# Kernel optimization log

Measured on AMD Instinct MI355X. Metric: run time of the kernel, lower is better.

## Reference

```python
import jax, jax.numpy as jnp
import numpy as np

B, T, C, HS = 4, 2048, 1024, 128

def setup_inputs() -> dict:
    key = jax.random.key(0)
    k0, k1, k2, k3 = jax.random.split(key, 4)
    scale = 1.0 / np.sqrt(C)
    return {
        "x": jax.random.normal(k0, (B, T, C), dtype=jnp.float32),
        "Wk": jax.random.normal(k1, (C, HS), dtype=jnp.float32) * scale,
        "Wq": jax.random.normal(k2, (C, HS), dtype=jnp.float32) * scale,
        "Wv": jax.random.normal(k3, (C, HS), dtype=jnp.float32) * scale,
    }

def reference(x, Wk, Wq, Wv):
    # k, q, v: [B, T, HS]
    k = jnp.einsum('btc,ch->bth', x, Wk)
    q = jnp.einsum('btc,ch->bth', x, Wq)
    v = jnp.einsum('btc,ch->bth', x, Wv)
    hs = k.shape[-1]
    # full T x T scores (no causal mask in source), scaled by head_size**-0.5
    wei = jnp.einsum('bqh,bkh->bqk', q, k) * (hs ** -0.5)
    wei = jax.nn.softmax(wei, axis=-1)
    # dropout p=0.0 -> identity
    out = jnp.einsum('bqk,bkh->bqh', wei, v)
    return out
```

## Files before the change

### kernel.cpp

```cpp
#include <hip/hip_runtime.h>
#include <hip/hip_bf16.h>

typedef float  f32x4  __attribute__((ext_vector_type(4)));
typedef float  f32x8  __attribute__((ext_vector_type(8)));
typedef float  f32x16 __attribute__((ext_vector_type(16)));
typedef short  s4v    __attribute__((ext_vector_type(4)));
typedef short  s8v    __attribute__((ext_vector_type(8)));
typedef __bf16 b4v    __attribute__((ext_vector_type(4)));
typedef __bf16 b8v    __attribute__((ext_vector_type(8)));
typedef unsigned int u32;
typedef unsigned short ushort;

#define T_DIM  2048
#define C_DIM  1024


typedef const __attribute__((address_space(1))) u32 gu32;
typedef __attribute__((address_space(3))) u32 lu32;

static __device__ __forceinline__ void glds16(const void* g, void* l) {
  __builtin_amdgcn_global_load_lds((gu32*)g, (lu32*)l, 16, 0, 0);
}

static __device__ __forceinline__ b8v ldb8(const ushort* p) {
  return __builtin_bit_cast(b8v, *reinterpret_cast<const s8v*>(p));
}

static __device__ __forceinline__ b4v cvt4(f32x4 v) {
  b4v r;
#pragma unroll
  for (int i = 0; i < 4; ++i) r[i] = (__bf16)v[i];
  return r;
}

static __device__ __forceinline__ ushort bfu(float f) {
  __bf16 h = (__bf16)f;
  return __builtin_bit_cast(ushort, h);
}

static __device__ __forceinline__ f32x16 mfma32(b8v a, b8v b, f32x16 c) {
  return __builtin_amdgcn_mfma_f32_32x32x16_bf16(a, b, c, 0, 0, 0);
}

#define BAR_VM(N)                                                        \
  asm volatile("s_waitcnt vmcnt(" #N ") lgkmcnt(0)" ::: "memory");       \
  __builtin_amdgcn_s_barrier();                                          \
  asm volatile("" ::: "memory");

__global__ __launch_bounds__(256) void wconv(const float* __restrict__ Wq,
                                             const float* __restrict__ Wk,
                                             const float* __restrict__ Wv,
                                             ushort* __restrict__ Wt) {
  __shared__ float lds[32][65];
  const int m  = blockIdx.z;
  const int c0 = blockIdx.x * 32;
  const int h0 = blockIdx.y * 64;
  const float* W = (m == 0) ? Wq : (m == 1) ? Wk : Wv;

  const int cl = threadIdx.x >> 3;
  const int h8 = (threadIdx.x & 7) * 8;
  {
    float4 a = *reinterpret_cast<const float4*>(W + (c0 + cl) * 128 + h0 + h8);
    float4 b =
        *reinterpret_cast<const float4*>(W + (c0 + cl) * 128 + h0 + h8 + 4);
    lds[cl][h8] = a.x; lds[cl][h8 + 1] = a.y;
    lds[cl][h8 + 2] = a.z; lds[cl][h8 + 3] = a.w;
    lds[cl][h8 + 4] = b.x; lds[cl][h8 + 5] = b.y;
    lds[cl][h8 + 6] = b.z; lds[cl][h8 + 7] = b.w;
  }
  __syncthreads();
  const int hl = threadIdx.x >> 2;
  const int cs = (threadIdx.x & 3) * 8;
  s8v o;
#pragma unroll
  for (int i = 0; i < 8; ++i) o[i] = (short)bfu(lds[cs + i][hl]);
  *reinterpret_cast<s8v*>(Wt + (m * 128 + h0 + hl) * C_DIM + c0 + cs) = o;
}

__global__ __launch_bounds__(512) void proj(const float* __restrict__ x,
                                            const ushort* __restrict__ Wt,
                                            ushort* __restrict__ q,
                                            ushort* __restrict__ k,
                                            ushort* __restrict__ vt) {
  __shared__ __align__(16) ushort Ab[2][32 * 72];
  __shared__ __align__(16) ushort Bb[2][128 * 64];
  float* red = (float*)&Bb[0][0];
  ushort* stage = &Bb[1][0];

  const int t   = threadIdx.x;
  const int w   = t >> 6;
  const int lid = t & 63;
  const int hi  = lid >> 5;
  const int ln  = lid & 31;
  const int ks  = w >> 2;
  const int nc  = w & 3;
  const int m   = blockIdx.y;
  const int r0  = blockIdx.x * 32;

  const int arow = t >> 4;
  const int acol = (t & 15) * 4;
  const float* ag = x + (r0 + arow) * C_DIM + acol;

  const int bswz = (((lid & 7) ^ (lid >> 3)) << 4);
  const char* bg = (const char*)(Wt + m * 128 * C_DIM);

  f32x16 acc[2] = {};

#define PROJ_BSTAGE(KK, BUF)                                              \
  _Pragma("unroll") for (int j = 0; j < 2; ++j) {                         \
    int h = j * 64 + w * 8 + (lid >> 3);                                  \
    glds16(bg + h * 2048 + (KK) * 2 + bswz,                               \
           (char*)&Bb[BUF][0] + j * 8192 + w * 1024);                     \
  }

  f32x4 av = *reinterpret_cast<const f32x4*>(ag);
  PROJ_BSTAGE(0, 0)
  {
    b4v ac = cvt4(av);
    *reinterpret_cast<s4v*>(&Ab[0][arow * 72 + acol]) =
        __builtin_bit_cast(s4v, ac);
  }
  __syncthreads();

  int cur = 0;
#pragma unroll 1
  for (int i = 0; i < 16; ++i) {
    const int nxt = cur ^ 1;
    f32x4 an;
    if (i < 15) {
      const int kk = (i + 1) * 64;
      PROJ_BSTAGE(kk, nxt)
      an = *reinterpret_cast<const f32x4*>(ag + kk);
    }

    const int h = nc * 32 + ln;
#pragma unroll
    for (int c = 0; c < 2; ++c) {
      const int s = ks * 2 + c;
      b8v af = ldb8(&Ab[cur][ln * 72 + s * 16 + hi * 8]);
      int inner = ((s * 2 + hi) << 4) ^ ((h & 7) << 4);
      b8v bf =
          ldb8((const ushort*)((const char*)&Bb[cur][0] + h * 128 + inner));
      __builtin_amdgcn_s_setprio(1);
      acc[c] = mfma32(af, bf, acc[c]);
      __builtin_amdgcn_s_setprio(0);
    }

    if (i < 15) {
      b4v anc = cvt4(an);
      *reinterpret_cast<s4v*>(&Ab[nxt][arow * 72 + acol]) =
          __builtin_bit_cast(s4v, anc);
    }
    __syncthreads();
    cur = nxt;
  }
#undef PROJ_BSTAGE

  f32x16 fa = acc[0] + acc[1];

  if (ks == 1) {
#pragma unroll
    for (int r = 0; r < 16; ++r) {
      int qm = (r & 3) + 8 * (r >> 2) + 4 * hi;
      red[(nc * 32 + qm) * 32 + ln] = fa[r];
    }
  }
  __syncthreads();
  if (ks == 0) {
#pragma unroll
    for (int r = 0; r < 16; ++r) {
      int qm = (r & 3) + 8 * (r >> 2) + 4 * hi;
      fa[r] += red[(nc * 32 + qm) * 32 + ln];
    }
    if (m < 2) {
#pragma unroll
      for (int r = 0; r < 16; ++r) {
        int row = (r & 3) + 8 * (r >> 2) + 4 * hi;
        stage[row * 136 + nc * 32 + ln] = bfu(fa[r]);
      }
    } else {
#pragma unroll
      for (int r = 0; r < 16; ++r) {
        int trow = (r & 3) + 8 * (r >> 2) + 4 * hi;
        stage[(nc * 32 + ln) * 40 + trow] = bfu(fa[r]);
      }
    }
  }
  __syncthreads();

  if (m < 2) {
    ushort* dst = (m == 0) ? q : k;
    int row = t >> 4, col8 = t & 15;
    s8v v8 = *reinterpret_cast<const s8v*>(&stage[row * 136 + col8 * 8]);
    *reinterpret_cast<s8v*>(&dst[(r0 + row) * 128 + col8 * 8]) = v8;
  } else {
    int b = blockIdx.x >> 6;
    int tbase = (blockIdx.x & 63) * 32;
    int h2 = t >> 2, t8 = t & 3;
    s8v v8 = *reinterpret_cast<const s8v*>(&stage[h2 * 40 + t8 * 8]);
    *reinterpret_cast<s8v*>(&vt[(b * 128 + h2) * T_DIM + tbase + t8 * 8]) = v8;
  }
}

#define ATTN_STAGE(KV0, BUF)                                              \
  _Pragma("unroll") for (int j = 0; j < 4; ++j) {                         \
    int row = w * 16 + j * 4 + (lid >> 4);                                \
    int p_ = (row >> 2) & 7;                                              \
    int pg = (p_ & 4) | ((p_ & 1) << 1) | ((p_ >> 1) & 1);                \
    int srow = (row & ~31) | (pg << 2) | (row & 3);                       \
    glds16(kgb + ((KV0) + srow) * 256 + (((lid & 15) ^ (row & 15)) << 4), \
           smem + (BUF) * 65536 + w * 4096 + j * 1024);                   \
  }                                                                       \
  _Pragma("unroll") for (int j = 0; j < 4; ++j) {                         \
    int h = w * 16 + j * 4 + (lid >> 4);                                  \
    glds16(vgb + h * 4096 + (KV0) * 2 + (((lid & 15) ^ (h & 15)) << 4),   \
           smem + (BUF) * 65536 + 32768 + w * 4096 + j * 1024);           \
  }

__global__ __launch_bounds__(512) void attn2(const ushort* __restrict__ q,
                                             const ushort* __restrict__ k,
                                             const ushort* __restrict__ vt,
                                             float* __restrict__ out,
                                             float* __restrict__ parts,
                                             float* __restrict__ lps) {
  extern __shared__ __align__(16) char smem[];

  const int t   = threadIdx.x;
  const int w   = t >> 6;
  const int lid = t & 63;
  const int hi  = lid >> 5;
  const int ln  = lid & 31;
  const int wq  = w >> 2;
  const int wk  = w & 3;

  const int id = blockIdx.x;
  const int g  = id & 7;
  const int b  = g >> 1;
  const int z  = g & 1;
  const int t0 = (id >> 3) * 64;

  const ushort* qp = q + (b * T_DIM + t0 + wq * 32) * 128;
  b8v aq[8];
#pragma unroll
  for (int s = 0; s < 8; ++s)
    aq[s] = ldb8(&qp[ln * 128 + s * 16 + hi * 8]);

  const char* kgb = (const char*)(k + b * T_DIM * 128);
  const char* vgb = (const char*)(vt + b * 128 * T_DIM);
  const int kv_base = z * 1024;

  const int R = wk * 32 + ln;
  int koff[8];
#pragma unroll
  for (int s = 0; s < 8; ++s)
    koff[s] = R * 256 + (((s * 2 + hi) ^ (R & 15)) << 4);
  int voff[4][2];
#pragma unroll
  for (int ht = 0; ht < 4; ++ht)
#pragma unroll
    for (int s = 0; s < 2; ++s) {
      int Hrow = ht * 32 + ln;
      int chunk = wk * 4 + s * 2 + hi;
      voff[ht][s] = 32768 + Hrow * 256 + ((chunk ^ (Hrow & 15)) << 4);
    }

  f32x16 of[4] = {};
  float lsum = 0.0f;
  const float scale = 0.08838834764831845f;

#define ATTN2_BODY(BUF)                                                  \
  {                                                                      \
    const char* Tb = smem + (BUF) * 65536;                               \
    b8v kfr[8];                                                          \
    _Pragma("unroll") for (int s = 0; s < 8; ++s)                        \
        kfr[s] = ldb8((const ushort*)(Tb + koff[s]));                    \
    f32x16 S = {};                                                       \
    __builtin_amdgcn_s_setprio(1);                                       \
    _Pragma("unroll") for (int s = 0; s < 8; ++s)                        \
        S = mfma32(kfr[s], aq[s], S);                                    \
    __builtin_amdgcn_s_setprio(0);                                       \
    float p[16];                                                         \
    _Pragma("unroll") for (int r = 0; r < 16; ++r) {                     \
      p[r] = __expf(S[r] * scale - 4.0f);                                \
      lsum += p[r];                                                      \
    }                                                                    \
    b8v pk0, pk1;                                                        \
    _Pragma("unroll") for (int r = 0; r < 8; ++r) {                      \
      pk0[r] = (__bf16)p[r];                                             \
      pk1[r] = (__bf16)p[8 + r];                                         \
    }                                                                    \
    __builtin_amdgcn_s_setprio(1);                                       \
    _Pragma("unroll") for (int ht = 0; ht < 4; ++ht) {                   \
      b8v v0 = ldb8((const ushort*)(Tb + voff[ht][0]));                  \
      b8v v1 = ldb8((const ushort*)(Tb + voff[ht][1]));                  \
      of[ht] = mfma32(pk0, v0, of[ht]);                                  \
      of[ht] = mfma32(pk1, v1, of[ht]);                                  \
    }                                                                    \
    __builtin_amdgcn_s_setprio(0);                                       \
  }

  ATTN_STAGE(kv_base, 0)

#pragma unroll 1
  for (int i = 0; i < 8; ++i) {
    BAR_VM(0)
    if (i < 7) { ATTN_STAGE(kv_base + (i + 1) * 128, (i + 1) & 1) }
    ATTN2_BODY(i & 1)
  }
#undef ATTN2_BODY

  lsum += __shfl_xor(lsum, 32);

  __syncthreads();

  float* ob = (float*)smem;
  float* lb = (float*)(smem + 98304);

  if (lid < 32) lb[(wq * 4 + wk) * 32 + lid] = lsum;
  if (wk != 0) {
#pragma unroll
    for (int ht = 0; ht < 4; ++ht)
#pragma unroll
      for (int r = 0; r < 16; ++r) {
        int qm = (r & 3) + 8 * (r >> 2) + 4 * hi;
        ob[((wk - 1) * 64 + wq * 32 + qm) * 128 + ht * 32 + ln] = of[ht][r];
      }
  }
  __syncthreads();
  if (wk == 0) {
    float* dsto = (z == 0) ? out : parts;
#pragma unroll
    for (int ht = 0; ht < 4; ++ht)
#pragma unroll
      for (int r = 0; r < 16; ++r) {
        int qm = (r & 3) + 8 * (r >> 2) + 4 * hi;
        int row = wq * 32 + qm;
        int col = ht * 32 + ln;
        float val = of[ht][r] + ob[(0 * 64 + row) * 128 + col] +
                    ob[(1 * 64 + row) * 128 + col] +
                    ob[(2 * 64 + row) * 128 + col];
        dsto[(b * T_DIM + t0 + row) * 128 + col] = val;
      }
    if (lid < 32) {
      float lt = lb[(wq * 4 + 0) * 32 + lid] + lb[(wq * 4 + 1) * 32 + lid] +
                 lb[(wq * 4 + 2) * 32 + lid] + lb[(wq * 4 + 3) * 32 + lid];
      lps[z * 8192 + b * T_DIM + t0 + wq * 32 + lid] = lt;
    }
  }
}

__global__ __launch_bounds__(256) void fin(float* __restrict__ out,
                                           const float* __restrict__ parts,
                                           const float* __restrict__ lps) {
  int tid = blockIdx.x * 256 + threadIdx.x;
  int idx = tid * 4;
  int row = idx >> 7;
  float inv = 1.0f / (lps[row] + lps[8192 + row]);
  f32x4 a = *reinterpret_cast<const f32x4*>(out + idx);
  f32x4 c = *reinterpret_cast<const f32x4*>(parts + idx);
  f32x4 r;
#pragma unroll
  for (int i = 0; i < 4; ++i) r[i] = (a[i] + c[i]) * inv;
  *reinterpret_cast<f32x4*>(out + idx) = r;
}

extern "C" void kernel_launch(void* const* d_in, const int* in_sizes, int n_in,
                              void* d_out, int out_size, void* d_ws,
                              size_t ws_size, hipStream_t stream) {
  const float* x  = (const float*)d_in[0];
  const float* Wk = (const float*)d_in[1];
  const float* Wq = (const float*)d_in[2];
  const float* Wv = (const float*)d_in[3];
  float* out = (float*)d_out;

  char* ws = (char*)d_ws;
  ushort* Wt  = (ushort*)ws;
  ushort* qb  = (ushort*)(ws + (1u << 20));
  ushort* kb  = (ushort*)(ws + 3u * (1u << 20));
  ushort* vtb = (ushort*)(ws + 5u * (1u << 20));
  float* parts = (float*)(ws + 8u * (1u << 20));
  float* lps   = (float*)(ws + 12u * (1u << 20));

  (void)hipFuncSetAttribute(reinterpret_cast<const void*>(&attn2),
                            hipFuncAttributeMaxDynamicSharedMemorySize, 131072);

  wconv<<<dim3(32, 2, 3), dim3(256), 0, stream>>>(Wq, Wk, Wv, Wt);
  proj<<<dim3(256, 3), dim3(512), 0, stream>>>(x, Wt, qb, kb, vtb);
  attn2<<<dim3(256), dim3(512), 131072, stream>>>(qb, kb, vtb, out,
                                                  parts, lps);
  fin<<<dim3(1024), dim3(256), 0, stream>>>(out, parts, lps);
}
```

Measured before the change: 48.05 us.

## Add 4-way KV split attention kernel with smaller tiles and finer barrier pipelining

Adds attn3, which splits the KV sequence four ways instead of two and uses 64-key stages with 64KB of LDS, launched as a 32x4x4 grid. Each warp also splits the head dimension so two warps share a key slice. This is meant to raise occupancy and CU coverage. Both attention kernels now split each iteration into a QK phase and a PV phase, with partial vmcnt waits so staged K can be consumed before V lands. The fin kernel is generalized to reduce nz partials, at the cost of more partial-output traffic. Which kernel runs depends on the workspace size, with attn2 kept as a fallback.

```diff
diff --git a/kernel.cpp b/kernel.cpp
--- a/kernel.cpp
+++ b/kernel.cpp
@@ -217,58 +217,7 @@
            smem + (BUF) * 65536 + 32768 + w * 4096 + j * 1024);           \
   }
 
-__global__ __launch_bounds__(512) void attn2(const ushort* __restrict__ q,
-                                             const ushort* __restrict__ k,
-                                             const ushort* __restrict__ vt,
-                                             float* __restrict__ out,
-                                             float* __restrict__ parts,
-                                             float* __restrict__ lps) {
-  extern __shared__ __align__(16) char smem[];
-
-  const int t   = threadIdx.x;
-  const int w   = t >> 6;
-  const int lid = t & 63;
-  const int hi  = lid >> 5;
-  const int ln  = lid & 31;
-  const int wq  = w >> 2;
-  const int wk  = w & 3;
-
-  const int id = blockIdx.x;
-  const int g  = id & 7;
-  const int b  = g >> 1;
-  const int z  = g & 1;
-  const int t0 = (id >> 3) * 64;
-
-  const ushort* qp = q + (b * T_DIM + t0 + wq * 32) * 128;
-  b8v aq[8];
-#pragma unroll
-  for (int s = 0; s < 8; ++s)
-    aq[s] = ldb8(&qp[ln * 128 + s * 16 + hi * 8]);
-
-  const char* kgb = (const char*)(k + b * T_DIM * 128);
-  const char* vgb = (const char*)(vt + b * 128 * T_DIM);
-  const int kv_base = z * 1024;
-
-  const int R = wk * 32 + ln;
-  int koff[8];
-#pragma unroll
-  for (int s = 0; s < 8; ++s)
-    koff[s] = R * 256 + (((s * 2 + hi) ^ (R & 15)) << 4);
-  int voff[4][2];
-#pragma unroll
-  for (int ht = 0; ht < 4; ++ht)
-#pragma unroll
-    for (int s = 0; s < 2; ++s) {
-      int Hrow = ht * 32 + ln;
-      int chunk = wk * 4 + s * 2 + hi;
-      voff[ht][s] = 32768 + Hrow * 256 + ((chunk ^ (Hrow & 15)) << 4);
-    }
-
-  f32x16 of[4] = {};
-  float lsum = 0.0f;
-  const float scale = 0.08838834764831845f;
-
-#define ATTN2_BODY(BUF)                                                  \
+#define ATTN2_QK(BUF)                                                    \
   {                                                                      \
     const char* Tb = smem + (BUF) * 65536;                               \
     b8v kfr[8];                                                          \
@@ -284,30 +233,91 @@
       p[r] = __expf(S[r] * scale - 4.0f);                                \
       lsum += p[r];                                                      \
     }                                                                    \
-    b8v pk0, pk1;                                                        \
     _Pragma("unroll") for (int r = 0; r < 8; ++r) {                      \
       pk0[r] = (__bf16)p[r];                                             \
       pk1[r] = (__bf16)p[8 + r];                                         \
     }                                                                    \
-    __builtin_amdgcn_s_setprio(1);                                       \
-    _Pragma("unroll") for (int ht = 0; ht < 4; ++ht) {                   \
-      b8v v0 = ldb8((const ushort*)(Tb + voff[ht][0]));                  \
-      b8v v1 = ldb8((const ushort*)(Tb + voff[ht][1]));                  \
-      of[ht] = mfma32(pk0, v0, of[ht]);                                  \
-      of[ht] = mfma32(pk1, v1, of[ht]);                                  \
-    }                                                                    \
-    __builtin_amdgcn_s_setprio(0);                                       \
-  }
+  }
+
+#define ATTN2_PV(BUF)                                                   \
+  {                                                                     \
+    const char* Tb = smem + (BUF) * 65536;                              \
+    __builtin_amdgcn_s_setprio(1);                                      \
+    _Pragma("unroll") for (int ht = 0; ht < 4; ++ht) {                  \
+      b8v v0 = ldb8((const ushort*)(Tb + voff[ht][0]));                 \
+      b8v v1 = ldb8((const ushort*)(Tb + voff[ht][1]));                 \
+      of[ht] = mfma32(pk0, v0, of[ht]);                                 \
+      of[ht] = mfma32(pk1, v1, of[ht]);                                 \
+    }                                                                   \
+    __builtin_amdgcn_s_setprio(0);                                      \
+  }
+
+__global__ __launch_bounds__(512) void attn2(const ushort* __restrict__ q,
+                                             const ushort* __restrict__ k,
+                                             const ushort* __restrict__ vt,
+                                             float* __restrict__ out,
+                                             float* __restrict__ parts,
+                                             float* __restrict__ lps) {
+  extern __shared__ __align__(16) char smem[];
+
+  const int t   = threadIdx.x;
+  const int w   = t >> 6;
+  const int lid = t & 63;
+  const int hi  = lid >> 5;
+  const int ln  = lid & 31;
+  const int wq  = w >> 2;
+  const int wk  = w & 3;
+
+  const int id = blockIdx.x;
+  const int g  = id & 7;
+  const int b  = g >> 1;
+  const int z  = g & 1;
+  const int t0 = (id >> 3) * 64;
+
+  const ushort* qp = q + (b * T_DIM + t0 + wq * 32) * 128;
+  b8v aq[8];
+#pragma unroll
+  for (int s = 0; s < 8; ++s)
+    aq[s] = ldb8(&qp[ln * 128 + s * 16 + hi * 8]);
+
+  const char* kgb = (const char*)(k + b * T_DIM * 128);
+  const char* vgb = (const char*)(vt + b * 128 * T_DIM);
+  const int kv_base = z * 1024;
+
+  const int R = wk * 32 + ln;
+  int koff[8];
+#pragma unroll
+  for (int s = 0; s < 8; ++s)
+    koff[s] = R * 256 + (((s * 2 + hi) ^ (R & 15)) << 4);
+  int voff[4][2];
+#pragma unroll
+  for (int ht = 0; ht < 4; ++ht)
+#pragma unroll
+    for (int s = 0; s < 2; ++s) {
+      int Hrow = ht * 32 + ln;
+      int chunk = wk * 4 + s * 2 + hi;
+      voff[ht][s] = 32768 + Hrow * 256 + ((chunk ^ (Hrow & 15)) << 4);
+    }
+
+  f32x16 of[4] = {};
+  float lsum = 0.0f;
+  b8v pk0, pk1;
+  const float scale = 0.08838834764831845f;
 
   ATTN_STAGE(kv_base, 0)
 
 #pragma unroll 1
-  for (int i = 0; i < 8; ++i) {
-    BAR_VM(0)
-    if (i < 7) { ATTN_STAGE(kv_base + (i + 1) * 128, (i + 1) & 1) }
-    ATTN2_BODY(i & 1)
-  }
-#undef ATTN2_BODY
+  for (int i = 0; i < 7; ++i) {
+    BAR_VM(4)
+    ATTN_STAGE(kv_base + (i + 1) * 128, (i + 1) & 1)
+    ATTN2_QK(i & 1)
+    BAR_VM(8)
+    ATTN2_PV(i & 1)
+  }
+  BAR_VM(4)
+  ATTN2_QK(1)
+  BAR_VM(0)
+  ATTN2_PV(1)
 
   lsum += __shfl_xor(lsum, 32);
 
@@ -349,18 +359,180 @@
   }
 }
 
+__global__ __launch_bounds__(512) void attn3(const ushort* __restrict__ q,
+                                             const ushort* __restrict__ k,
+                                             const ushort* __restrict__ vt,
+                                             float* __restrict__ out,
+                                             float* __restrict__ parts,
+                                             float* __restrict__ lps) {
+  extern __shared__ __align__(16) char smem[];
+
+  const int t   = threadIdx.x;
+  const int w   = t >> 6;
+  const int lid = t & 63;
+  const int hi  = lid >> 5;
+  const int ln  = lid & 31;
+  const int wq  = w >> 2;
+  const int wh  = (w >> 1) & 1;
+  const int wk  = w & 1;
+  const int b   = blockIdx.y;
+  const int z   = blockIdx.z;
+  const int t0  = blockIdx.x * 64;
+
+  const ushort* qp = q + (b * T_DIM + t0 + wq * 32) * 128;
+  b8v aq[8];
+#pragma unroll
+  for (int s = 0; s < 8; ++s)
+    aq[s] = ldb8(&qp[ln * 128 + s * 16 + hi * 8]);
+
+  const char* kgb = (const char*)(k + b * T_DIM * 128);
+  const char* vgb = (const char*)(vt + b * 128 * T_DIM);
+  const int kv_base = z * 512;
+
+  const int R = wk * 32 + ln;
+  int koff[8];
+#pragma unroll
+  for (int s = 0; s < 8; ++s)
+    koff[s] = R * 256 + (((s * 2 + hi) ^ (R & 15)) << 4);
+  int voff[2][2];
+#pragma unroll
+  for (int ht = 0; ht < 2; ++ht)
+#pragma unroll
+    for (int s = 0; s < 2; ++s) {
+      int Hrow = wh * 64 + ht * 32 + ln;
+      int chunk = wk * 4 + s * 2 + hi;
+      voff[ht][s] = 16384 + Hrow * 128 + ((chunk ^ (Hrow & 7)) << 4);
+    }
+
+  f32x16 of[2] = {};
+  float lsum = 0.0f;
+  b8v pk0, pk1;
+  const float scale = 0.08838834764831845f;
+
+#define A3_STAGE(KV0, BUF)                                                \
+  _Pragma("unroll") for (int j = 0; j < 2; ++j) {                         \
+    int row = (w * 2 + j) * 4 + (lid >> 4);                               \
+    int p_ = (row >> 2) & 7;                                              \
+    int pg = (p_ & 4) | ((p_ & 1) << 1) | ((p_ >> 1) & 1);                \
+    int srow = (row & ~31) | (pg << 2) | (row & 3);                       \
+    glds16(kgb + ((KV0) + srow) * 256 + (((lid & 15) ^ (row & 15)) << 4), \
+           smem + (BUF) * 32768 + (w * 2 + j) * 1024);                    \
+  }                                                                       \
+  _Pragma("unroll") for (int j = 0; j < 2; ++j) {                         \
+    int h = (w * 2 + j) * 8 + (lid >> 3);                                 \
+    glds16(vgb + h * 4096 + (KV0) * 2 + (((lid & 7) ^ (h & 7)) << 4),     \
+           smem + (BUF) * 32768 + 16384 + (w * 2 + j) * 1024);            \
+  }
+
+#define A3_QK(BUF)                                                       \
+  {                                                                      \
+    const char* Tb = smem + (BUF) * 32768;                               \
+    b8v kfr[8];                                                          \
+    _Pragma("unroll") for (int s = 0; s < 8; ++s)                        \
+        kfr[s] = ldb8((const ushort*)(Tb + koff[s]));                    \
+    f32x16 S = {};                                                       \
+    __builtin_amdgcn_s_setprio(1);                                       \
+    _Pragma("unroll") for (int s = 0; s < 8; ++s)                        \
+        S = mfma32(kfr[s], aq[s], S);                                    \
+    __builtin_amdgcn_s_setprio(0);                                       \
+    float p[16];                                                         \
+    _Pragma("unroll") for (int r = 0; r < 16; ++r) {                     \
+      p[r] = __expf(S[r] * scale - 4.0f);                                \
+      lsum += p[r];                                                      \
+    }                                                                    \
+    _Pragma("unroll") for (int r = 0; r < 8; ++r) {                      \
+      pk0[r] = (__bf16)p[r];                                             \
+      pk1[r] = (__bf16)p[8 + r];                                         \
+    }                                                                    \
+  }
+
+#define A3_PV(BUF)                                                      \
+  {                                                                     \
+    const char* Tb = smem + (BUF) * 32768;                              \
+    __builtin_amdgcn_s_setprio(1);                                      \
+    _Pragma("unroll") for (int ht = 0; ht < 2; ++ht) {                  \
+      b8v v0 = ldb8((const ushort*)(Tb + voff[ht][0]));                 \
+      b8v v1 = ldb8((const ushort*)(Tb + voff[ht][1]));                 \
+      of[ht] = mfma32(pk0, v0, of[ht]);                                 \
+      of[ht] = mfma32(pk1, v1, of[ht]);                                 \
+    }                                                                   \
+    __builtin_amdgcn_s_setprio(0);                                      \
+  }
+
+  A3_STAGE(kv_base, 0)
+
+#pragma unroll 1
+  for (int i = 0; i < 7; ++i) {
+    BAR_VM(2)
+    A3_STAGE(kv_base + (i + 1) * 64, (i + 1) & 1)
+    A3_QK(i & 1)
+    BAR_VM(4)
+    A3_PV(i & 1)
+  }
+  BAR_VM(2)
+  A3_QK(1)
+  BAR_VM(0)
+  A3_PV(1)
+
+#undef A3_STAGE
+#undef A3_QK
+#undef A3_PV
+
+  lsum += __shfl_xor(lsum, 32);
+
+  __syncthreads();
+
+  float* ob = (float*)smem;
+  float* lb = (float*)(smem + 32768);
+
+  if (wh == 0 && lid < 32) lb[(wk * 2 + wq) * 32 + lid] = lsum;
+  if (wk == 1) {
+#pragma unroll
+    for (int ht = 0; ht < 2; ++ht)
+#pragma unroll
+      for (int r = 0; r < 16; ++r) {
+        int qm = (r & 3) + 8 * (r >> 2) + 4 * hi;
+        ob[(wq * 2 + wh) * 2048 + qm * 64 + ht * 32 + ln] = of[ht][r];
+      }
+  }
+  __syncthreads();
+  if (wk == 0) {
+    float* dsto = (z == 0) ? out : (parts + (z - 1) * 1048576);
+#pragma unroll
+    for (int ht = 0; ht < 2; ++ht)
+#pragma unroll
+      for (int r = 0; r < 16; ++r) {
+        int qm = (r & 3) + 8 * (r >> 2) + 4 * hi;
+        int row = wq * 32 + qm;
+        int col = wh * 64 + ht * 32 + ln;
+        float val = of[ht][r] + ob[(wq * 2 + wh) * 2048 + qm * 64 + ht * 32 + ln];
+        dsto[(b * T_DIM + t0 + row) * 128 + col] = val;
+      }
+    if (wh == 0 && lid < 32) {
+      float lt = lb[(0 * 2 + wq) * 32 + lid] + lb[(1 * 2 + wq) * 32 + lid];
+      lps[z * 8192 + b * T_DIM + t0 + wq * 32 + lid] = lt;
+    }
+  }
+}
+
 __global__ __launch_bounds__(256) void fin(float* __restrict__ out,
                                            const float* __restrict__ parts,
-                                           const float* __restrict__ lps) {
+                                           const float* __restrict__ lps,
+                                           int nz) {
   int tid = blockIdx.x * 256 + threadIdx.x;
   int idx = tid * 4;
   int row = idx >> 7;
-  float inv = 1.0f / (lps[row] + lps[8192 + row]);
+  float l = lps[row];
+  for (int zz = 1; zz < nz; ++zz) l += lps[zz * 8192 + row];
+  float inv = 1.0f / l;
   f32x4 a = *reinterpret_cast<const f32x4*>(out + idx);
-  f32x4 c = *reinterpret_cast<const f32x4*>(parts + idx);
+  for (int zz = 1; zz < nz; ++zz) {
+    f32x4 c = *reinterpret_cast<const f32x4*>(parts + (zz - 1) * 1048576 + idx);
+    a += c;
+  }
   f32x4 r;
 #pragma unroll
-  for (int i = 0; i < 4; ++i) r[i] = (a[i] + c[i]) * inv;
+  for (int i = 0; i < 4; ++i) r[i] = a[i] * inv;
   *reinterpret_cast<f32x4*>(out + idx) = r;
 }
 
@@ -375,18 +547,29 @@
 
   char* ws = (char*)d_ws;
   ushort* Wt  = (ushort*)ws;
-  ushort* qb  = (ushort*)(ws + (1u << 20));
-  ushort* kb  = (ushort*)(ws + 3u * (1u << 20));
-  ushort* vtb = (ushort*)(ws + 5u * (1u << 20));
-  float* parts = (float*)(ws + 8u * (1u << 20));
-  float* lps   = (float*)(ws + 12u * (1u << 20));
+  ushort* qb  = (ushort*)(ws + 786432);
+  ushort* kb  = (ushort*)(ws + 2883584);
+  ushort* vtb = (ushort*)(ws + 4980736);
+  float* parts = (float*)(ws + 7077888);
+
+  const bool big = ws_size >= 19800000u;
+  float* lps = big ? (float*)(ws + 7077888 + 3u * 4194304u)
+                   : (float*)(ws + 7077888 + 4194304u);
 
   (void)hipFuncSetAttribute(reinterpret_cast<const void*>(&attn2),
                             hipFuncAttributeMaxDynamicSharedMemorySize, 131072);
+  (void)hipFuncSetAttribute(reinterpret_cast<const void*>(&attn3),
+                            hipFuncAttributeMaxDynamicSharedMemorySize, 65536);
 
   wconv<<<dim3(32, 2, 3), dim3(256), 0, stream>>>(Wq, Wk, Wv, Wt);
   proj<<<dim3(256, 3), dim3(512), 0, stream>>>(x, Wt, qb, kb, vtb);
-  attn2<<<dim3(256), dim3(512), 131072, stream>>>(qb, kb, vtb, out,
-                                                  parts, lps);
-  fin<<<dim3(1024), dim3(256), 0, stream>>>(out, parts, lps);
-}
+  if (big) {
+    attn3<<<dim3(32, 4, 4), dim3(512), 65536, stream>>>(qb, kb, vtb, out,
+                                                        parts, lps);
+    fin<<<dim3(1024), dim3(256), 0, stream>>>(out, parts, lps, 4);
+  } else {
+    attn2<<<dim3(256), dim3(512), 131072, stream>>>(qb, kb, vtb, out,
+                                                    parts, lps);
+    fin<<<dim3(1024), dim3(256), 0, stream>>>(out, parts, lps, 2);
+  }
+}
```

After: 55.11 us. +14.7%, slower.
